# Kernel optimization log

Measured on AMD Instinct MI355X. Metric: run time of the kernel, lower is better.

Reference implementation:

```python
import math
import jax, jax.numpy as jnp
import numpy as np

NUM_HEADS = 32

def _alibi_slopes(n: int) -> jnp.ndarray:
    cp2 = 2 ** int(math.floor(math.log2(n)))
    base = 2.0 ** (-(2.0 ** (-(math.log2(cp2) - 3))))
    slopes = base ** np.arange(1, cp2 + 1, dtype=np.float64)
    if cp2 != n:
        extra_base = 2.0 ** (-(2.0 ** (-(math.log2(2 * cp2) - 3))))
        rem = min(cp2, n - cp2)
        slopes = np.concatenate([slopes, extra_base ** np.arange(1, 1 + 2 * rem, 2, dtype=np.float64)])
    return jnp.asarray(slopes, dtype=jnp.float32)


def setup_inputs() -> dict:
    key = jax.random.key(0)
    k1, k2, k3 = jax.random.split(key, 3)
    B, S, E, H, D = 2, 2048, 4096, NUM_HEADS, 128
    hidden_states = jax.random.normal(k1, (B, S, E), dtype=jnp.float32)
    # torch Linear y = x @ W^T; we store transposed weights [in, out]
    w_qkv = jax.random.normal(k2, (E, H * D + 2 * D), dtype=jnp.float32) * 0.02
    w_c = jax.random.normal(k3, (E, E), dtype=jnp.float32) * 0.02
    return {"hidden_states": hidden_states, "w_qkv": w_qkv, "w_c": w_c}


def reference(hidden_states, w_qkv, w_c):
    B, S, E = hidden_states.shape
    H = NUM_HEADS
    D = E // H
    scaling = D ** -0.5

    qkv = hidden_states @ w_qkv                      # [B,S,H*D+2D]
    q = qkv[..., : H * D].reshape(B, S, H, D)        # [B,S,H,D]
    k = qkv[..., H * D: H * D + D]                   # [B,S,D] single KV head (MQA)
    v = qkv[..., H * D + D:]                         # [B,S,D]

    pos = jnp.arange(S)
    slopes = _alibi_slopes(H)                        # [H]
    # ALiBi: slope * (k_pos - q_pos), <= 0 in the causal region
    bias = slopes[:, None, None] * (pos[None, None, :] - pos[None, :, None]).astype(jnp.float32)  # [H,S,S]

    scores = jnp.einsum('bqhd,bkd->bhqk', q, k) * scaling + bias[None]  # [B,H,S,S]
    causal = pos[:, None] >= pos[None, :]            # [S,S]
    scores = jnp.where(causal[None, None], scores, jnp.finfo(scores.dtype).min)
    probs = jax.nn.softmax(scores, axis=-1)
    attn = jnp.einsum('bhqk,bkd->bqhd', probs, v).reshape(B, S, E)
    return attn @ w_c
```

## Files before the change

### kernel.cpp

```cpp
#include <hip/hip_runtime.h>
#include <hip/hip_bf16.h>

typedef unsigned short u16;
typedef unsigned int u32;
typedef __attribute__((ext_vector_type(8))) short s16x8;
typedef __attribute__((ext_vector_type(4))) float f32x4;

#define MFMA_BF16(a, b, c) __builtin_amdgcn_mfma_f32_16x16x32_bf16(a, b, c, 0, 0, 0)

__device__ __forceinline__ u16 f2bf(float f) {
  union { float f; u32 u; } c; c.f = f;
  return (u16)((c.u + 0x7FFFu + ((c.u >> 16) & 1u)) >> 16);
}

__device__ __forceinline__ u32 pkbf(float a, float b) {
  float2 t; t.x = a; t.y = b;
  __hip_bfloat162 h = __float22bfloat162_rn(t);
  union { __hip_bfloat162 h; u32 u; } c; c.h = h; return c.u;
}

__device__ __forceinline__ void gll16(const void* g, void* l) {
  __builtin_amdgcn_global_load_lds((const __attribute__((address_space(1))) void*)g,
                                   (__attribute__((address_space(3))) void*)l, 16, 0, 0);
}

__device__ __forceinline__ f32x4 f4zero() { f32x4 z = {0.f, 0.f, 0.f, 0.f}; return z; }

__global__ void cvt_bf16_kernel(const float4* __restrict__ in, u16* __restrict__ out, int n4) {
  int i = blockIdx.x * 256 + threadIdx.x;
  if (i >= n4) return;
  float4 v = in[i];
  uint2 w;
  w.x = (u32)f2bf(v.x) | ((u32)f2bf(v.y) << 16);
  w.y = (u32)f2bf(v.z) | ((u32)f2bf(v.w) << 16);
  *reinterpret_cast<uint2*>(out + (size_t)i * 4) = w;
}

__global__ void transpose_cvt_kernel(const float* __restrict__ in, u16* __restrict__ out,
                                     int R, int C) {
  __shared__ float tile[32][33];
  int tx = threadIdx.x, ty = threadIdx.y;
  int r0 = blockIdx.y * 32, c0 = blockIdx.x * 32;
#pragma unroll
  for (int i = 0; i < 32; i += 8)
    tile[ty + i][tx] = in[(size_t)(r0 + ty + i) * C + c0 + tx];
  __syncthreads();
#pragma unroll
  for (int i = 0; i < 32; i += 8)
    out[(size_t)(c0 + ty + i) * R + r0 + tx] = f2bf(tile[tx][ty + i]);
}


#define PHASE(QM, QN, PR, STAGE_STMT, WAIT_STMT) do {                                   \
  s16x8 af[4][2], bb[2][2];                                                             \
  _Pragma("unroll")                                                                     \
  for (int mi2 = 0; mi2 < 4; ++mi2) {                                                   \
    af[mi2][0] = *(const s16x8*)(smem + (PR)*32768 + (QM)*16384 + mi2*2048 + aOff0);    \
    af[mi2][1] = *(const s16x8*)(smem + (PR)*32768 + (QM)*16384 + mi2*2048 + aOff1);    \
  }                                                                                     \
  _Pragma("unroll")                                                                     \
  for (int ni2 = 0; ni2 < 2; ++ni2) {                                                   \
    bb[ni2][0] = *(const s16x8*)(smem + 65536 + (PR)*32768 + (QN)*16384 + ni2*2048 + bOff0); \
    bb[ni2][1] = *(const s16x8*)(smem + 65536 + (PR)*32768 + (QN)*16384 + ni2*2048 + bOff1); \
  }                                                                                     \
  STAGE_STMT;                                                                           \
  WAIT_STMT;                                                                            \
  __builtin_amdgcn_s_barrier();                                                         \
  asm volatile("s_waitcnt lgkmcnt(0)" ::: "memory");                                    \
  __builtin_amdgcn_s_setprio(1);                                                        \
  _Pragma("unroll")                                                                     \
  for (int ks = 0; ks < 2; ++ks)                                                        \
    _Pragma("unroll")                                                                   \
    for (int mi2 = 0; mi2 < 4; ++mi2)                                                   \
      _Pragma("unroll")                                                                 \
      for (int ni2 = 0; ni2 < 2; ++ni2)                                                 \
        acc[(QM)*4 + mi2][(QN)*2 + ni2] =                                               \
            MFMA_BF16(af[mi2][ks], bb[ni2][ks], acc[(QM)*4 + mi2][(QN)*2 + ni2]);       \
  __builtin_amdgcn_s_setprio(0);                                                        \
  __builtin_amdgcn_s_barrier();                                                         \
} while (0)

#define STAGE_PAIR(x, PW, kn) do {                                                      \
  gll16(srcA[x] + (kn), smem + (PW)*32768 + (x)*8192 + tt*16);                          \
  gll16(srcB[x] + (kn), smem + 65536 + (PW)*32768 + (x)*8192 + tt*16);                  \
} while (0)

#define VM3 asm volatile("s_waitcnt vmcnt(3)" ::: "memory")
#define VM4 asm volatile("s_waitcnt vmcnt(4)" ::: "memory")
#define VM1 asm volatile("s_waitcnt vmcnt(1)" ::: "memory")
#define VM0 asm volatile("s_waitcnt vmcnt(0)" ::: "memory")
#define NOPSTMT do {} while (0)

#define TILE_MAIN(PR, PW, kn) do {                                                      \
  PHASE(0, 0, PR, STAGE_PAIR(0, PW, kn), VM3);                                          \
  PHASE(1, 0, PR, STAGE_PAIR(1, PW, kn), VM4);                                          \
  PHASE(0, 1, PR, STAGE_PAIR(2, PW, kn), NOPSTMT);                                      \
  PHASE(1, 1, PR, STAGE_PAIR(3, PW, kn), VM4);                                          \
} while (0)

#define TILE_LAST(PR) do {                                                              \
  PHASE(0, 0, PR, NOPSTMT, VM1);                                                        \
  PHASE(1, 0, PR, NOPSTMT, VM0);                                                        \
  PHASE(0, 1, PR, NOPSTMT, NOPSTMT);                                                    \
  PHASE(1, 1, PR, NOPSTMT, NOPSTMT);                                                    \
} while (0)

template<int EPI>
__global__ __launch_bounds__(512, 2)
void gemm256_kernel(const u16* __restrict__ A, const u16* __restrict__ Bt,
                    float* __restrict__ Cf, u16* __restrict__ Cq,
                    u16* __restrict__ Ck, u16* __restrict__ Cvt,
                    int N, int K) {
  __shared__ __align__(16) char smem[131072];
  const int tt = threadIdx.x;
  const int w = tt >> 6, l = tt & 63;
  const int li = l & 15, g = l >> 4;
  const int wm = w >> 2, wn = w & 3;

  const int gx = gridDim.x;
  const int nwg = gx * gridDim.y;
  int id = blockIdx.y * gx + blockIdx.x;
  id = (id & 7) * (nwg >> 3) + (id >> 3);
  const int bn = id % gx, bm = id / gx;

  f32x4 acc[8][4];
#pragma unroll
  for (int i = 0; i < 8; ++i)
#pragma unroll
    for (int j = 0; j < 4; ++j) acc[i][j] = f4zero();

  const int q8 = (((tt & 7) ^ ((tt >> 3) & 7)) * 8);
  const u16* srcA[4];
  const u16* srcB[4];
#pragma unroll
  for (int x = 0; x < 4; ++x) {
    const int arow = (x & 1) * 128 + (x >> 1) * 64 + (tt >> 3);
    srcA[x] = A + (size_t)(bm * 256 + arow) * K + q8;
    const int rho = x * 64 + (tt >> 3);
    const int qn_ = rho >> 7, rem = rho & 127;
    const int wn_ = rem >> 5, rr = rem & 31;
    const int brow = wn_ * 64 + qn_ * 32 + rr;
    srcB[x] = Bt + (size_t)(bn * 256 + brow) * K + q8;
  }

  const int gr0 = (g ^ (li & 7)) * 16;
  const int aOff0 = wm * 8192 + li * 128 + gr0;
  const int aOff1 = aOff0 ^ 64;
  const int bOff0 = wn * 4096 + li * 128 + gr0;
  const int bOff1 = bOff0 ^ 64;

#pragma unroll
  for (int x = 0; x < 4; ++x) STAGE_PAIR(x, 0, 0);
  VM4;
  __builtin_amdgcn_s_barrier();

  for (int t2 = 0; t2 < 62; t2 += 2) {
    TILE_MAIN(0, 1, (t2 + 1) * 64);
    TILE_MAIN(1, 0, (t2 + 2) * 64);
  }
  TILE_MAIN(0, 1, 63 * 64);
  TILE_LAST(1);

#pragma unroll
  for (int mi = 0; mi < 8; ++mi) {
#pragma unroll
    for (int ni = 0; ni < 4; ++ni) {
      const int row0 = bm * 256 + wm * 128 + mi * 16 + g * 4;
      const int col = bn * 256 + wn * 64 + ni * 16 + li;
#pragma unroll
      for (int r = 0; r < 4; ++r) {
        const int m = row0 + r;
        const float v = acc[mi][ni][r];
        if (EPI == 0) {
          Cf[(size_t)m * N + col] = v;
        } else {
          const int bb2 = m >> 11, s = m & 2047;
          const int kt = s >> 5;
          const size_t tb = (size_t)(bb2 * 64 + kt);
          if (col < 4096) {
            Cq[(size_t)m * 4096 + col] = f2bf(v);
          } else if (col < 4224) {
            const int d = col - 4096, kr = s & 31;
            const int mk = kr >> 4, lii = kr & 15;
            const int kk = d >> 5, gg = (d >> 3) & 3, e = d & 7;
            Ck[(tb * 8 + mk * 4 + kk) * 512 + (gg * 16 + lii) * 8 + e] = f2bf(v);
          } else {
            const int d = col - 4224, kp = s & 31;
            const int mf = d >> 4, lii = d & 15;
            const int gg = kp >> 3, e = kp & 7;
            Cvt[(tb * 8 + mf) * 512 + (gg * 16 + lii) * 8 + e] = f2bf(v);
          }
        }
      }
    }
  }
}


__device__ __forceinline__ void load_ktile(s16x8 (&dst)[8], const u16* kf, size_t tb, int l) {
#pragma unroll
  for (int f = 0; f < 8; ++f)
    dst[f] = *(const s16x8*)&kf[(tb * 8 + f) * 512 + l * 8];
}

template<bool DIAG>
__device__ __forceinline__ void attn_tile(
    int kt, const u16* kf, const u16* vf, size_t bb64, int l, int li, int g,
    s16x8 (&use)[8], s16x8 (&fill)[8], bool do_fill,
    const s16x8 (&bq)[2][4], f32x4 (&acc)[8][2],
    float (&m_)[2], float (&lp)[2], float (&bias)[2],
    float c1, const float (&cjr)[8], float bstep, u16 (*Pw)[40]) {
  const size_t tb = bb64 + kt;
  s16x8 vr[8];
#pragma unroll
  for (int f = 0; f < 8; ++f)
    vr[f] = *(const s16x8*)&vf[(tb * 8 + f) * 512 + l * 8];
  if (do_fill) load_ktile(fill, kf, tb - 1, l);

  f32x4 sc[2][2];
  sc[0][0] = f4zero(); sc[0][1] = f4zero(); sc[1][0] = f4zero(); sc[1][1] = f4zero();
#pragma unroll
  for (int kk = 0; kk < 4; ++kk)
#pragma unroll
    for (int mk = 0; mk < 2; ++mk) {
      sc[mk][0] = MFMA_BF16(use[mk * 4 + kk], bq[0][kk], sc[mk][0]);
      sc[mk][1] = MFMA_BF16(use[mk * 4 + kk], bq[1][kk], sc[mk][1]);
    }

#pragma unroll
  for (int nq = 0; nq < 2; ++nq) {
    float sv[8];
    float pm = -3e38f;
    if (DIAG) {
#pragma unroll
      for (int mk = 0; mk < 2; ++mk)
#pragma unroll
        for (int r = 0; r < 4; ++r) {
          const int kd = mk * 16 + g * 4 + r - (nq * 16 + li);
          float s = fmaf(sc[mk][nq][r], c1, bias[nq] + cjr[mk * 4 + r]);
          s = (kd <= 0) ? s : -1e30f;
          sv[mk * 4 + r] = s;
          pm = fmaxf(pm, s);
        }
      pm = fmaxf(pm, __shfl_xor(pm, 16));
      pm = fmaxf(pm, __shfl_xor(pm, 32));
      m_[nq] = pm;
    } else {
#pragma unroll
      for (int mk = 0; mk < 2; ++mk)
#pragma unroll
        for (int r = 0; r < 4; ++r) {
          float s = fmaf(sc[mk][nq][r], c1, bias[nq] + cjr[mk * 4 + r]);
          sv[mk * 4 + r] = s;
          pm = fmaxf(pm, s);
        }
      if (__any(pm > m_[nq])) {
        pm = fmaxf(pm, __shfl_xor(pm, 16));
        pm = fmaxf(pm, __shfl_xor(pm, 32));
        const float nm = fmaxf(m_[nq], pm);
        const float scale = exp2f(m_[nq] - nm);
#pragma unroll
        for (int mf = 0; mf < 8; ++mf) acc[mf][nq] *= scale;
        lp[nq] *= scale;
        m_[nq] = nm;
      }
    }
    const float mref = m_[nq];
    float e[8];
#pragma unroll
    for (int j = 0; j < 8; ++j) e[j] = exp2f(sv[j] - mref);
    lp[nq] += ((e[0] + e[1]) + (e[2] + e[3])) + ((e[4] + e[5]) + (e[6] + e[7]));
#pragma unroll
    for (int mk = 0; mk < 2; ++mk) {
      uint2 wv;
      wv.x = pkbf(e[mk * 4 + 0], e[mk * 4 + 1]);
      wv.y = pkbf(e[mk * 4 + 2], e[mk * 4 + 3]);
      *reinterpret_cast<uint2*>(&Pw[nq * 16 + li][mk * 16 + g * 4]) = wv;
    }
    bias[nq] -= bstep;
  }

  s16x8 pb0 = *(const s16x8*)&Pw[li][g * 8];
  s16x8 pb1 = *(const s16x8*)&Pw[16 + li][g * 8];
#pragma unroll
  for (int mf = 0; mf < 8; ++mf) {
    acc[mf][0] = MFMA_BF16(vr[mf], pb0, acc[mf][0]);
    acc[mf][1] = MFMA_BF16(vr[mf], pb1, acc[mf][1]);
  }
}

__device__ __forceinline__ void attn_qtile(
    int qt, int h, int b, const u16* qbuf, const u16* kf, const u16* vf,
    u16* obuf, int l, int li, int g, float c1, float sl2, u16 (*Pw)[40]) {
  const int S = 2048;
  const int q0 = qt * 32;
  const size_t bb64 = (size_t)b * 64;

  s16x8 bq[2][4];
#pragma unroll
  for (int nq = 0; nq < 2; ++nq)
#pragma unroll
    for (int kk = 0; kk < 4; ++kk)
      bq[nq][kk] = *(const s16x8*)&qbuf[(size_t)(b * S + q0 + nq * 16 + li) * 4096
                                        + h * 128 + kk * 32 + g * 8];

  f32x4 acc[8][2];
#pragma unroll
  for (int mf = 0; mf < 8; ++mf) { acc[mf][0] = f4zero(); acc[mf][1] = f4zero(); }
  float m_[2] = {-3e38f, -3e38f};
  float lp[2] = {0.f, 0.f};

  float cjr[8];
#pragma unroll
  for (int j = 0; j < 8; ++j) cjr[j] = sl2 * (float)((j >> 2) * 16 + (j & 3));
  float bias[2];
#pragma unroll
  for (int nq = 0; nq < 2; ++nq)
    bias[nq] = sl2 * (float)(g * 4 - nq * 16 - li);
  const float bstep = sl2 * 32.f;

  s16x8 kA[8], kB[8];
  load_ktile(kA, kf, bb64 + qt, l);
  attn_tile<true>(qt, kf, vf, bb64, l, li, g, kA, kB, qt >= 1,
                  bq, acc, m_, lp, bias, c1, cjr, bstep, Pw);
  int kt = qt - 1;
  while (kt >= 1) {
    attn_tile<false>(kt, kf, vf, bb64, l, li, g, kB, kA, true,
                     bq, acc, m_, lp, bias, c1, cjr, bstep, Pw);
    attn_tile<false>(kt - 1, kf, vf, bb64, l, li, g, kA, kB, kt >= 2,
                     bq, acc, m_, lp, bias, c1, cjr, bstep, Pw);
    kt -= 2;
  }
  if (kt == 0)
    attn_tile<false>(0, kf, vf, bb64, l, li, g, kB, kA, false,
                     bq, acc, m_, lp, bias, c1, cjr, bstep, Pw);

#pragma unroll
  for (int nq = 0; nq < 2; ++nq) {
    float ls = lp[nq];
    ls += __shfl_xor(ls, 16);
    ls += __shfl_xor(ls, 32);
    const float inv = 1.f / ls;
    const size_t rowbase = (size_t)(b * S + q0 + nq * 16 + li) * 4096 + h * 128;
#pragma unroll
    for (int mf = 0; mf < 8; ++mf) {
      f32x4 v = acc[mf][nq];
      uint2 wv;
      wv.x = pkbf(v[0] * inv, v[1] * inv);
      wv.y = pkbf(v[2] * inv, v[3] * inv);
      *reinterpret_cast<uint2*>(&obuf[rowbase + mf * 16 + g * 4]) = wv;
    }
  }
}

__global__ __launch_bounds__(64, 2)
void attn_kernel(const u16* __restrict__ qbuf, const u16* __restrict__ kf,
                 const u16* __restrict__ vf, u16* __restrict__ obuf) {
  const int p = blockIdx.x, h = blockIdx.y, b = blockIdx.z;
  const int l = threadIdx.x, li = l & 15, g = l >> 4;
  const float L2E = 1.4426950408889634f;
  const float slope = exp2f(-0.25f * (float)(h + 1));
  const float c1 = 0.08838834764831845f * L2E;
  const float sl2 = slope * L2E;
  __shared__ __align__(16) u16 P[32][40];
  attn_qtile(63 - p, h, b, qbuf, kf, vf, obuf, l, li, g, c1, sl2, P);
  attn_qtile(p, h, b, qbuf, kf, vf, obuf, l, li, g, c1, sl2, P);
}

extern "C" void kernel_launch(void* const* d_in, const int* in_sizes, int n_in,
                              void* d_out, int out_size, void* d_ws, size_t ws_size,
                              hipStream_t stream) {
  (void)in_sizes; (void)n_in; (void)out_size; (void)ws_size;
  const float* hidden = (const float*)d_in[0];
  const float* w_qkv = (const float*)d_in[1];
  const float* w_c = (const float*)d_in[2];
  float* out = (float*)d_out;
  char* ws = (char*)d_ws;

  u16* hid_bf = (u16*)(ws + 0);
  u16* wT     = (u16*)(ws + 33554432);
  u16* qbuf   = (u16*)(ws + 69206016);
  u16* kbuf   = (u16*)(ws + 102760448);
  u16* vtbuf  = (u16*)(ws + 103809024);

  cvt_bf16_kernel<<<16384, 256, 0, stream>>>((const float4*)hidden, hid_bf, 4194304);
  transpose_cvt_kernel<<<dim3(136, 128), dim3(32, 8), 0, stream>>>(w_qkv, wT, 4096, 4352);
  gemm256_kernel<1><<<dim3(17, 16), 512, 0, stream>>>(hid_bf, wT, nullptr, qbuf, kbuf, vtbuf,
                                                      4352, 4096);
  attn_kernel<<<dim3(32, 32, 2), 64, 0, stream>>>(qbuf, kbuf, vtbuf, hid_bf);
  transpose_cvt_kernel<<<dim3(128, 128), dim3(32, 8), 0, stream>>>(w_c, wT, 4096, 4096);
  gemm256_kernel<0><<<dim3(16, 16), 512, 0, stream>>>(hid_bf, wT, out, nullptr, nullptr, nullptr,
                                                      4096, 4096);
}
```

Before: 531.1 us.

## Reorder GEMM quadrant phases to reuse A/B fragments across phases

Restructures the 256x256 bf16 GEMM main loop so the four quadrant phases run in a snake order (00, 01, 11, 10). Each A or B register fragment is then reused by consecutive phases instead of being reloaded from LDS every phase, which cuts LDS read traffic. Global-to-LDS staging is regrouped into two halves with matching vmcnt waits, and the prologue now waits for every load to finish. The cost is more live fragment registers on top of the large accumulator set, which raises register pressure and the risk of spills.

Measured after the change: 503.9 us. 1.05x faster.

```diff
diff --git a/kernel.cpp b/kernel.cpp
--- a/kernel.cpp
+++ b/kernel.cpp
@@ -51,59 +51,64 @@
 }
 
 
-#define PHASE(QM, QN, PR, STAGE_STMT, WAIT_STMT) do {                                   \
-  s16x8 af[4][2], bb[2][2];                                                             \
-  _Pragma("unroll")                                                                     \
-  for (int mi2 = 0; mi2 < 4; ++mi2) {                                                   \
-    af[mi2][0] = *(const s16x8*)(smem + (PR)*32768 + (QM)*16384 + mi2*2048 + aOff0);    \
-    af[mi2][1] = *(const s16x8*)(smem + (PR)*32768 + (QM)*16384 + mi2*2048 + aOff1);    \
-  }                                                                                     \
-  _Pragma("unroll")                                                                     \
-  for (int ni2 = 0; ni2 < 2; ++ni2) {                                                   \
-    bb[ni2][0] = *(const s16x8*)(smem + 65536 + (PR)*32768 + (QN)*16384 + ni2*2048 + bOff0); \
-    bb[ni2][1] = *(const s16x8*)(smem + 65536 + (PR)*32768 + (QN)*16384 + ni2*2048 + bOff1); \
-  }                                                                                     \
-  STAGE_STMT;                                                                           \
-  WAIT_STMT;                                                                            \
-  __builtin_amdgcn_s_barrier();                                                         \
-  asm volatile("s_waitcnt lgkmcnt(0)" ::: "memory");                                    \
-  __builtin_amdgcn_s_setprio(1);                                                        \
-  _Pragma("unroll")                                                                     \
-  for (int ks = 0; ks < 2; ++ks)                                                        \
-    _Pragma("unroll")                                                                   \
-    for (int mi2 = 0; mi2 < 4; ++mi2)                                                   \
-      _Pragma("unroll")                                                                 \
-      for (int ni2 = 0; ni2 < 2; ++ni2)                                                 \
-        acc[(QM)*4 + mi2][(QN)*2 + ni2] =                                               \
-            MFMA_BF16(af[mi2][ks], bb[ni2][ks], acc[(QM)*4 + mi2][(QN)*2 + ni2]);       \
-  __builtin_amdgcn_s_setprio(0);                                                        \
-  __builtin_amdgcn_s_barrier();                                                         \
-} while (0)
-
-#define STAGE_PAIR(x, PW, kn) do {                                                      \
-  gll16(srcA[x] + (kn), smem + (PW)*32768 + (x)*8192 + tt*16);                          \
-  gll16(srcB[x] + (kn), smem + 65536 + (PW)*32768 + (x)*8192 + tt*16);                  \
-} while (0)
-
-#define VM3 asm volatile("s_waitcnt vmcnt(3)" ::: "memory")
+#define BARRIER __builtin_amdgcn_s_barrier()
+#define LGKM0 asm volatile("s_waitcnt lgkmcnt(0)" ::: "memory")
+#define PRIO1 __builtin_amdgcn_s_setprio(1)
+#define PRIO0 __builtin_amdgcn_s_setprio(0)
 #define VM4 asm volatile("s_waitcnt vmcnt(4)" ::: "memory")
-#define VM1 asm volatile("s_waitcnt vmcnt(1)" ::: "memory")
 #define VM0 asm volatile("s_waitcnt vmcnt(0)" ::: "memory")
 #define NOPSTMT do {} while (0)
 
-#define TILE_MAIN(PR, PW, kn) do {                                                      \
-  PHASE(0, 0, PR, STAGE_PAIR(0, PW, kn), VM3);                                          \
-  PHASE(1, 0, PR, STAGE_PAIR(1, PW, kn), VM4);                                          \
-  PHASE(0, 1, PR, STAGE_PAIR(2, PW, kn), NOPSTMT);                                      \
-  PHASE(1, 1, PR, STAGE_PAIR(3, PW, kn), VM4);                                          \
+#define RD_A(dst, PR, QM) do { _Pragma("unroll")                                         \
+  for (int mi2 = 0; mi2 < 4; ++mi2) {                                                    \
+    dst[mi2][0] = *(const s16x8*)(smem + (PR)*32768 + (QM)*16384 + mi2*2048 + aOff0);    \
+    dst[mi2][1] = *(const s16x8*)(smem + (PR)*32768 + (QM)*16384 + mi2*2048 + aOff1);    \
+  } } while (0)
+
+#define RD_B(dst, PR, QN) do { _Pragma("unroll")                                         \
+  for (int ni2 = 0; ni2 < 2; ++ni2) {                                                    \
+    dst[ni2][0] = *(const s16x8*)(smem + 65536 + (PR)*32768 + (QN)*16384 + ni2*2048 + bOff0); \
+    dst[ni2][1] = *(const s16x8*)(smem + 65536 + (PR)*32768 + (QN)*16384 + ni2*2048 + bOff1); \
+  } } while (0)
+
+#define MFMA_Q(QM, QN, Af, Bf) do { _Pragma("unroll")                                    \
+  for (int ks = 0; ks < 2; ++ks) { _Pragma("unroll")                                     \
+    for (int mi2 = 0; mi2 < 4; ++mi2) { _Pragma("unroll")                                \
+      for (int ni2 = 0; ni2 < 2; ++ni2)                                                  \
+        acc[(QM)*4+mi2][(QN)*2+ni2] =                                                    \
+            MFMA_BF16(Af[mi2][ks], Bf[ni2][ks], acc[(QM)*4+mi2][(QN)*2+ni2]);            \
+  } } } while (0)
+
+#define STAGE_PAIR(x, PW, kn) do {                                                       \
+  gll16(srcA[x] + (kn), smem + (PW)*32768 + (x)*8192 + tt*16);                           \
+  gll16(srcB[x] + (kn), smem + 65536 + (PW)*32768 + (x)*8192 + tt*16);                   \
 } while (0)
 
-#define TILE_LAST(PR) do {                                                              \
-  PHASE(0, 0, PR, NOPSTMT, VM1);                                                        \
-  PHASE(1, 0, PR, NOPSTMT, VM0);                                                        \
-  PHASE(0, 1, PR, NOPSTMT, NOPSTMT);                                                    \
-  PHASE(1, 1, PR, NOPSTMT, NOPSTMT);                                                    \
+#define STAGE_H1(PW, kn) do { STAGE_PAIR(0, PW, kn); STAGE_PAIR(1, PW, kn); } while (0)
+#define STAGE_H2(PW, kn) do { STAGE_PAIR(2, PW, kn); STAGE_PAIR(3, PW, kn); } while (0)
+
+#define TILE_BODY(PR, ST1, ST2, W1, W4) do {                                             \
+  s16x8 a0[4][2], a1[4][2], b0[2][2], b1[2][2];                                          \
+                       \
+  RD_A(a0, PR, 0); RD_B(b0, PR, 0);                                                      \
+  ST1;                                                                                   \
+  BARRIER; LGKM0; PRIO1; MFMA_Q(0, 0, a0, b0); PRIO0;                                    \
+  W1; BARRIER;                                                                           \
+                            \
+  RD_B(b1, PR, 1);                                                                       \
+  ST2;                                                                                   \
+  BARRIER; LGKM0; PRIO1; MFMA_Q(0, 1, a0, b1); PRIO0; BARRIER;                           \
+                                                    \
+  RD_A(a1, PR, 1);                                                                       \
+  BARRIER; LGKM0; PRIO1; MFMA_Q(1, 1, a1, b1); PRIO0; BARRIER;                           \
+                                                 \
+  RD_B(b0, PR, 0);                                                                       \
+  BARRIER; LGKM0; PRIO1; MFMA_Q(1, 0, a1, b0); PRIO0;                                    \
+  W4; BARRIER;                                                                           \
 } while (0)
+
+#define TILE_MAIN(PR, PW, kn) TILE_BODY(PR, STAGE_H1(PW, kn), STAGE_H2(PW, kn), VM4, VM4)
+#define TILE_LAST(PR) TILE_BODY(PR, NOPSTMT, NOPSTMT, VM0, NOPSTMT)
 
 template<int EPI>
 __global__ __launch_bounds__(512, 2)
@@ -149,10 +154,10 @@
   const int bOff0 = wn * 4096 + li * 128 + gr0;
   const int bOff1 = bOff0 ^ 64;
 
-#pragma unroll
-  for (int x = 0; x < 4; ++x) STAGE_PAIR(x, 0, 0);
-  VM4;
-  __builtin_amdgcn_s_barrier();
+  STAGE_H1(0, 0);
+  STAGE_H2(0, 0);
+  VM0;
+  BARRIER;
 
   for (int t2 = 0; t2 < 62; t2 += 2) {
     TILE_MAIN(0, 1, (t2 + 1) * 64);
```
